# Performance work log

Measured on AMD Instinct MI355X. Metric: run time of the kernel, lower is better.

Reference implementation:

```python
import jax, jax.numpy as jnp
import numpy as np

# NaiveMatryoshkaLinear(dim=4096, hidden_dim=4096, heads=[8,8,16], bias=False)
# head_dim = 4096 // 32 = 128
# input_dims  (cumsum heads * head_dim) = [1024, 2048, 4096]
# output_dims (heads * head_dim)        = [1024, 1024, 2048]
INPUT_DIMS = (1024, 2048, 4096)
OUTPUT_DIMS = (1024, 1024, 2048)


def setup_inputs() -> dict:
    key = jax.random.key(0)
    kx, k0, k1, k2 = jax.random.split(key, 4)
    x = jax.random.normal(kx, (4, 4096, 4096), dtype=jnp.float32)
    # torch nn.Linear weight layout: (out_features, in_features), kaiming-uniform-ish init
    def init_w(k, out_d, in_d):
        bound = 1.0 / np.sqrt(in_d)
        return jax.random.uniform(k, (out_d, in_d), dtype=jnp.float32, minval=-bound, maxval=bound)
    W0 = init_w(k0, OUTPUT_DIMS[0], INPUT_DIMS[0])
    W1 = init_w(k1, OUTPUT_DIMS[1], INPUT_DIMS[1])
    W2 = init_w(k2, OUTPUT_DIMS[2], INPUT_DIMS[2])
    return {"x": x, "W0": W0, "W1": W1, "W2": W2}


def reference(x, W0, W1, W2):
    # Block-triangular matryoshka linear: each head i projects the prefix
    # x[..., :input_dims[i]] with its own weight, outputs are concatenated.
    y0 = jnp.einsum('bsd,od->bso', x[..., :INPUT_DIMS[0]], W0)
    y1 = jnp.einsum('bsd,od->bso', x[..., :INPUT_DIMS[1]], W1)
    y2 = jnp.einsum('bsd,od->bso', x[..., :INPUT_DIMS[2]], W2)
    return jnp.concatenate([y0, y1, y2], axis=-1)  # [4, 4096, 4096]
```

## Files before the change

### kernel.cpp

```cpp
#include <hip/hip_runtime.h>
#include <hip/hip_bf16.h>


typedef short bf16x8 __attribute__((ext_vector_type(8)));
typedef float f32x4 __attribute__((ext_vector_type(4)));

__device__ __forceinline__ ushort f2bf(float f) {
  union { float f; unsigned u; } c; c.f = f;
  unsigned u = c.u;
  unsigned r = u + 0x7fffu + ((u >> 16) & 1u);
  return (ushort)(r >> 16);
}

__global__ void cvt_all_bf16(const float* __restrict__ x,
                             const float* __restrict__ W0,
                             const float* __restrict__ W1,
                             const float* __restrict__ W2,
                             ushort* __restrict__ dst) {
  const int X4  = 16777216;
  const int E0  = X4 + 262144;
  const int E1  = E0 + 524288;
  const int E2  = E1 + 2097152;
  int i = blockIdx.x * blockDim.x + threadIdx.x;
  int stride = gridDim.x * blockDim.x;
  ushort4* out4 = (ushort4*)dst;
  for (int j = i; j < E2; j += stride) {
    const float4* src;
    if (j < X4)      src = (const float4*)x  + j;
    else if (j < E0) src = (const float4*)W0 + (j - X4);
    else if (j < E1) src = (const float4*)W1 + (j - E0);
    else             src = (const float4*)W2 + (j - E1);
    float4 v = *src;
    ushort4 o;
    o.x = f2bf(v.x); o.y = f2bf(v.y); o.z = f2bf(v.z); o.w = f2bf(v.w);
    out4[j] = o;
  }
}

__device__ __forceinline__ void gload16(const ushort* g, const ushort* l) {
  __builtin_amdgcn_global_load_lds(
      (const __attribute__((address_space(1))) void*)g,
      (__attribute__((address_space(3))) void*)l, 16, 0, 0);
}

#define TILE_E 8192

#define MF(av, bv, mi, ni) \
  acc[mi][ni] = __builtin_amdgcn_mfma_f32_16x16x32_bf16(av, bv, acc[mi][ni], 0, 0, 0)

__global__ __launch_bounds__(512, 2) void matry_gemm(
    const ushort* __restrict__ xbf,
    const ushort* __restrict__ w0,
    const ushort* __restrict__ w1,
    const ushort* __restrict__ w2,
    float* __restrict__ out) {
  __shared__ __align__(16) ushort sA[4][TILE_E];
  __shared__ __align__(16) ushort sB[4][TILE_E];

  const int bid = blockIdx.x;
  const int rt = bid & 63;
  const int ct = bid >> 6;

  int K; const ushort* W; int nl0;
  if (ct < 4)      { K = 1024; W = w0; nl0 = ct * 256; }
  else if (ct < 8) { K = 2048; W = w1; nl0 = (ct - 4) * 256; }
  else             { K = 4096; W = w2; nl0 = (ct - 8) * 256; }
  const int NT = K >> 5;
  const int m0 = rt * 256;
  const int n0 = ct * 256;

  const int tid  = threadIdx.x;
  const int wid  = tid >> 6;
  const int lane = tid & 63;
  const int wm = wid >> 2;
  const int wn = wid & 3;
  const int fr = lane & 15;
  const int swz_e = (((lane >> 4) ^ ((lane >> 1) & 3)) << 3);

  const int srow = tid >> 2;
  const int scol = (((tid & 3) ^ ((tid >> 3) & 3)) << 3);
  const ushort* Asrc0 = xbf + (size_t)(m0 + srow) * 4096 + scol;
  const ushort* Asrc1 = Asrc0 + (size_t)128 * 4096;
  const ushort* Bsrc0 = W + (size_t)(nl0 + srow) * K + scol;
  const ushort* Bsrc1 = Bsrc0 + (size_t)128 * K;
  const int d0 = tid * 8;
  const int d1 = 4096 + tid * 8;

  f32x4 acc[8][4];
#pragma unroll
  for (int mi = 0; mi < 8; ++mi)
#pragma unroll
    for (int ni = 0; ni < 4; ++ni)
      acc[mi][ni] = (f32x4){0.f, 0.f, 0.f, 0.f};

#pragma unroll
  for (int pt = 0; pt < 3; ++pt) {
    const int ks = pt * 32;
    gload16(Asrc0 + ks, &sA[pt][d0]);
    gload16(Asrc1 + ks, &sA[pt][d1]);
    gload16(Bsrc0 + ks, &sB[pt][d0]);
    gload16(Bsrc1 + ks, &sB[pt][d1]);
  }
  asm volatile("s_waitcnt vmcnt(8)" ::: "memory");
  __builtin_amdgcn_s_barrier();

  for (int t = 0; t < NT; ++t) {
    const int b = t & 3;
    const ushort* pa = &sA[b][(wm * 128 + fr) * 32 + swz_e];
    const ushort* pb = &sB[b][(wn * 64 + fr) * 32 + swz_e];
    const int ts = (t + 3 < NT) ? (t + 3) : (NT - 1);
    const int ks = ts << 5;
    const int bs = (t + 3) & 3;

    bf16x8 a0 = *(const bf16x8*)(pa);
    bf16x8 a1 = *(const bf16x8*)(pa + 512);
    bf16x8 a2 = *(const bf16x8*)(pa + 1024);
    bf16x8 a3 = *(const bf16x8*)(pa + 1536);
    bf16x8 b0 = *(const bf16x8*)(pb);
    bf16x8 b1 = *(const bf16x8*)(pb + 512);
    bf16x8 b2 = *(const bf16x8*)(pb + 1024);
    bf16x8 b3 = *(const bf16x8*)(pb + 1536);
    gload16(Asrc0 + ks, &sA[bs][d0]);
    gload16(Asrc1 + ks, &sA[bs][d1]);
    __builtin_amdgcn_s_setprio(1);
    MF(a0, b0, 0, 0); MF(a0, b1, 0, 1); MF(a0, b2, 0, 2); MF(a0, b3, 0, 3);
    MF(a1, b0, 1, 0); MF(a1, b1, 1, 1); MF(a1, b2, 1, 2); MF(a1, b3, 1, 3);
    MF(a2, b0, 2, 0); MF(a2, b1, 2, 1); MF(a2, b2, 2, 2); MF(a2, b3, 2, 3);
    MF(a3, b0, 3, 0); MF(a3, b1, 3, 1); MF(a3, b2, 3, 2); MF(a3, b3, 3, 3);
    __builtin_amdgcn_s_setprio(0);

    bf16x8 a4 = *(const bf16x8*)(pa + 2048);
    bf16x8 a5 = *(const bf16x8*)(pa + 2560);
    bf16x8 a6 = *(const bf16x8*)(pa + 3072);
    bf16x8 a7 = *(const bf16x8*)(pa + 3584);
    gload16(Bsrc0 + ks, &sB[bs][d0]);
    gload16(Bsrc1 + ks, &sB[bs][d1]);
    __builtin_amdgcn_s_setprio(1);
    MF(a4, b0, 4, 0); MF(a4, b1, 4, 1); MF(a4, b2, 4, 2); MF(a4, b3, 4, 3);
    MF(a5, b0, 5, 0); MF(a5, b1, 5, 1); MF(a5, b2, 5, 2); MF(a5, b3, 5, 3);
    MF(a6, b0, 6, 0); MF(a6, b1, 6, 1); MF(a6, b2, 6, 2); MF(a6, b3, 6, 3);
    MF(a7, b0, 7, 0); MF(a7, b1, 7, 1); MF(a7, b2, 7, 2); MF(a7, b3, 7, 3);
    __builtin_amdgcn_s_setprio(0);

    asm volatile("s_waitcnt vmcnt(8)" ::: "memory");
    __builtin_amdgcn_s_barrier();
  }

  const int rq = (lane >> 4) * 4;
#pragma unroll
  for (int mi = 0; mi < 8; ++mi) {
#pragma unroll
    for (int ni = 0; ni < 4; ++ni) {
      const int n = n0 + wn * 64 + ni * 16 + fr;
#pragma unroll
      for (int r = 0; r < 4; ++r) {
        const int m = m0 + wm * 128 + mi * 16 + rq + r;
        out[(size_t)m * 4096 + n] = acc[mi][ni][r];
      }
    }
  }
}

__global__ void naive_kernel(const float* __restrict__ x,
                             const float* __restrict__ W0,
                             const float* __restrict__ W1,
                             const float* __restrict__ W2,
                             float* __restrict__ out) {
  long idx = (long)blockIdx.x * 256 + threadIdx.x;
  int n = (int)(idx & 4095);
  long m = idx >> 12;
  int K; const float* W; int nl;
  if (n < 1024)      { K = 1024; W = W0; nl = n; }
  else if (n < 2048) { K = 2048; W = W1; nl = n - 1024; }
  else               { K = 4096; W = W2; nl = n - 2048; }
  const float* xr = x + m * 4096;
  const float* wr = W + (long)nl * K;
  float s = 0.f;
  for (int k = 0; k < K; ++k) s += xr[k] * wr[k];
  out[idx] = s;
}

extern "C" void kernel_launch(void* const* d_in, const int* in_sizes, int n_in,
                              void* d_out, int out_size, void* d_ws,
                              size_t ws_size, hipStream_t stream) {
  const float* x  = (const float*)d_in[0];
  const float* W0 = (const float*)d_in[1];
  const float* W1 = (const float*)d_in[2];
  const float* W2 = (const float*)d_in[3];
  float* out = (float*)d_out;

  const size_t xN  = (size_t)16384 * 4096;
  const size_t w0N = (size_t)1024 * 1024;
  const size_t w1N = (size_t)1024 * 2048;
  const size_t w2N = (size_t)2048 * 4096;
  const size_t need = (xN + w0N + w1N + w2N) * sizeof(ushort);

  if (ws_size >= need) {
    ushort* xbf = (ushort*)d_ws;
    ushort* w0b = xbf + xN;
    ushort* w1b = w0b + w0N;
    ushort* w2b = w1b + w1N;
    cvt_all_bf16<<<4096, 256, 0, stream>>>(x, W0, W1, W2, xbf);
    matry_gemm<<<1024, 512, 0, stream>>>(xbf, w0b, w1b, w2b, out);
  } else {
    naive_kernel<<<(int)((xN + 255) / 256), 256, 0, stream>>>(x, W0, W1, W2, out);
  }
}
```

Before: 451.4 us.

## Cut prefetch depth to two tiles and barrier once per two K-tiles

The GEMM main loop is unrolled by two, with a single workgroup barrier after each pair of K-tiles instead of after every tile. Prefetch distance drops from three tiles to two, with matching vmcnt waits, so a free slot in the four-buffer LDS ring allows the skipped barrier. The aim is to cut barrier stalls between waves. The costs are less latency hiding for global-to-LDS loads, and a visibility risk: the second tile of each pair is read after only a per-thread vmcnt wait, with no barrier guaranteeing other threads' LDS writes are done.

Measured after the change: 495.5 us. 1.1x slower.

```diff
diff --git a/kernel.cpp b/kernel.cpp
--- a/kernel.cpp
+++ b/kernel.cpp
@@ -48,6 +48,44 @@
 #define MF(av, bv, mi, ni) \
   acc[mi][ni] = __builtin_amdgcn_mfma_f32_16x16x32_bf16(av, bv, acc[mi][ni], 0, 0, 0)
 
+#define TILE_BODY(TT)                                                         \
+  {                                                                           \
+    const int b_ = (TT) & 3;                                                  \
+    const ushort* pa = &sA[b_][(wm * 128 + fr) * 32 + swz_e];                 \
+    const ushort* pb = &sB[b_][(wn * 64 + fr) * 32 + swz_e];                  \
+    const int ts_ = ((TT) + 2 < NT) ? ((TT) + 2) : (NT - 1);                  \
+    const int ks_ = ts_ << 5;                                                 \
+    const int bs_ = ((TT) + 2) & 3;                                           \
+    bf16x8 a0 = *(const bf16x8*)(pa);                                         \
+    bf16x8 a1 = *(const bf16x8*)(pa + 512);                                   \
+    bf16x8 a2 = *(const bf16x8*)(pa + 1024);                                  \
+    bf16x8 a3 = *(const bf16x8*)(pa + 1536);                                  \
+    bf16x8 b0 = *(const bf16x8*)(pb);                                         \
+    bf16x8 b1 = *(const bf16x8*)(pb + 512);                                   \
+    bf16x8 b2 = *(const bf16x8*)(pb + 1024);                                  \
+    bf16x8 b3 = *(const bf16x8*)(pb + 1536);                                  \
+    gload16(Asrc0 + ks_, &sA[bs_][d0]);                                       \
+    gload16(Asrc1 + ks_, &sA[bs_][d1]);                                       \
+    __builtin_amdgcn_s_setprio(1);                                            \
+    MF(a0, b0, 0, 0); MF(a0, b1, 0, 1); MF(a0, b2, 0, 2); MF(a0, b3, 0, 3);   \
+    MF(a1, b0, 1, 0); MF(a1, b1, 1, 1); MF(a1, b2, 1, 2); MF(a1, b3, 1, 3);   \
+    MF(a2, b0, 2, 0); MF(a2, b1, 2, 1); MF(a2, b2, 2, 2); MF(a2, b3, 2, 3);   \
+    MF(a3, b0, 3, 0); MF(a3, b1, 3, 1); MF(a3, b2, 3, 2); MF(a3, b3, 3, 3);   \
+    __builtin_amdgcn_s_setprio(0);                                            \
+    bf16x8 a4 = *(const bf16x8*)(pa + 2048);                                  \
+    bf16x8 a5 = *(const bf16x8*)(pa + 2560);                                  \
+    bf16x8 a6 = *(const bf16x8*)(pa + 3072);                                  \
+    bf16x8 a7 = *(const bf16x8*)(pa + 3584);                                  \
+    gload16(Bsrc0 + ks_, &sB[bs_][d0]);                                       \
+    gload16(Bsrc1 + ks_, &sB[bs_][d1]);                                       \
+    __builtin_amdgcn_s_setprio(1);                                            \
+    MF(a4, b0, 4, 0); MF(a4, b1, 4, 1); MF(a4, b2, 4, 2); MF(a4, b3, 4, 3);   \
+    MF(a5, b0, 5, 0); MF(a5, b1, 5, 1); MF(a5, b2, 5, 2); MF(a5, b3, 5, 3);   \
+    MF(a6, b0, 6, 0); MF(a6, b1, 6, 1); MF(a6, b2, 6, 2); MF(a6, b3, 6, 3);   \
+    MF(a7, b0, 7, 0); MF(a7, b1, 7, 1); MF(a7, b2, 7, 2); MF(a7, b3, 7, 3);   \
+    __builtin_amdgcn_s_setprio(0);                                            \
+  }
+
 __global__ __launch_bounds__(512, 2) void matry_gemm(
     const ushort* __restrict__ xbf,
     const ushort* __restrict__ w0,
@@ -94,55 +132,21 @@
       acc[mi][ni] = (f32x4){0.f, 0.f, 0.f, 0.f};
 
 #pragma unroll
-  for (int pt = 0; pt < 3; ++pt) {
+  for (int pt = 0; pt < 2; ++pt) {
     const int ks = pt * 32;
     gload16(Asrc0 + ks, &sA[pt][d0]);
     gload16(Asrc1 + ks, &sA[pt][d1]);
     gload16(Bsrc0 + ks, &sB[pt][d0]);
     gload16(Bsrc1 + ks, &sB[pt][d1]);
   }
-  asm volatile("s_waitcnt vmcnt(8)" ::: "memory");
+  asm volatile("s_waitcnt vmcnt(4)" ::: "memory");
   __builtin_amdgcn_s_barrier();
 
-  for (int t = 0; t < NT; ++t) {
-    const int b = t & 3;
-    const ushort* pa = &sA[b][(wm * 128 + fr) * 32 + swz_e];
-    const ushort* pb = &sB[b][(wn * 64 + fr) * 32 + swz_e];
-    const int ts = (t + 3 < NT) ? (t + 3) : (NT - 1);
-    const int ks = ts << 5;
-    const int bs = (t + 3) & 3;
-
-    bf16x8 a0 = *(const bf16x8*)(pa);
-    bf16x8 a1 = *(const bf16x8*)(pa + 512);
-    bf16x8 a2 = *(const bf16x8*)(pa + 1024);
-    bf16x8 a3 = *(const bf16x8*)(pa + 1536);
-    bf16x8 b0 = *(const bf16x8*)(pb);
-    bf16x8 b1 = *(const bf16x8*)(pb + 512);
-    bf16x8 b2 = *(const bf16x8*)(pb + 1024);
-    bf16x8 b3 = *(const bf16x8*)(pb + 1536);
-    gload16(Asrc0 + ks, &sA[bs][d0]);
-    gload16(Asrc1 + ks, &sA[bs][d1]);
-    __builtin_amdgcn_s_setprio(1);
-    MF(a0, b0, 0, 0); MF(a0, b1, 0, 1); MF(a0, b2, 0, 2); MF(a0, b3, 0, 3);
-    MF(a1, b0, 1, 0); MF(a1, b1, 1, 1); MF(a1, b2, 1, 2); MF(a1, b3, 1, 3);
-    MF(a2, b0, 2, 0); MF(a2, b1, 2, 1); MF(a2, b2, 2, 2); MF(a2, b3, 2, 3);
-    MF(a3, b0, 3, 0); MF(a3, b1, 3, 1); MF(a3, b2, 3, 2); MF(a3, b3, 3, 3);
-    __builtin_amdgcn_s_setprio(0);
-
-    bf16x8 a4 = *(const bf16x8*)(pa + 2048);
-    bf16x8 a5 = *(const bf16x8*)(pa + 2560);
-    bf16x8 a6 = *(const bf16x8*)(pa + 3072);
-    bf16x8 a7 = *(const bf16x8*)(pa + 3584);
-    gload16(Bsrc0 + ks, &sB[bs][d0]);
-    gload16(Bsrc1 + ks, &sB[bs][d1]);
-    __builtin_amdgcn_s_setprio(1);
-    MF(a4, b0, 4, 0); MF(a4, b1, 4, 1); MF(a4, b2, 4, 2); MF(a4, b3, 4, 3);
-    MF(a5, b0, 5, 0); MF(a5, b1, 5, 1); MF(a5, b2, 5, 2); MF(a5, b3, 5, 3);
-    MF(a6, b0, 6, 0); MF(a6, b1, 6, 1); MF(a6, b2, 6, 2); MF(a6, b3, 6, 3);
-    MF(a7, b0, 7, 0); MF(a7, b1, 7, 1); MF(a7, b2, 7, 2); MF(a7, b3, 7, 3);
-    __builtin_amdgcn_s_setprio(0);
-
-    asm volatile("s_waitcnt vmcnt(8)" ::: "memory");
+  for (int t = 0; t < NT; t += 2) {
+    TILE_BODY(t);
+    asm volatile("s_waitcnt vmcnt(4)" ::: "memory");
+    TILE_BODY(t + 1);
+    asm volatile("s_waitcnt vmcnt(4)" ::: "memory");
     __builtin_amdgcn_s_barrier();
   }
 
```
